# Performance work log

Measured on AMD Instinct MI355X. Metric: run time of the kernel, lower is better.

The kernel has to match this reference:

```python
import jax, jax.numpy as jnp
import numpy as np

B, S, D = 8, 1024, 1024
H, DH = 16, 64  # num_attention_heads, attention_head_size; H*DH == D


def setup_inputs() -> dict:
    key = jax.random.key(0)
    ks = jax.random.split(key, 6)
    scale = 0.02
    return {
        "hidden_states": jax.random.normal(ks[0], (B, S, D), jnp.float32),
        "right_hidden_states": jax.random.normal(ks[1], (B, S, D), jnp.float32),
        "attention_mask": jnp.ones((B, S, S), jnp.float32),
        "Wq": jax.random.normal(ks[2], (D, H * DH), jnp.float32) * scale,
        "bq": jnp.zeros((H * DH,), jnp.float32),
        "Wk": jax.random.normal(ks[3], (D, H * DH), jnp.float32) * scale,
        "bk": jnp.zeros((H * DH,), jnp.float32),
        "Wv": jax.random.normal(ks[4], (D, H * DH), jnp.float32) * scale,
        "bv": jnp.zeros((H * DH,), jnp.float32),
    }


def _split_heads(x, b):
    # (B, S, H*DH) -> (B, H, S, DH)
    return x.reshape(b, -1, H, DH).transpose(0, 2, 1, 3)


def reference(hidden_states, right_hidden_states, attention_mask, Wq, bq, Wk, bk, Wv, bv):
    b = hidden_states.shape[0]
    q = _split_heads(hidden_states @ Wq + bq, b)          # (B,H,Sq,DH)
    k = _split_heads(right_hidden_states @ Wk + bk, b)    # (B,H,Sk,DH)
    v = _split_heads(right_hidden_states @ Wv + bv, b)    # (B,H,Sk,DH)

    scores = jnp.einsum("bhqd,bhkd->bhqk", q, k) / jnp.sqrt(jnp.asarray(DH, q.dtype))
    scores = jnp.sum(scores, axis=1, keepdims=True)       # (B,1,Sq,Sk) head-summed

    ext = (1.0 - attention_mask[:, None, :, :].astype(scores.dtype)) * -1e9
    probs = jax.nn.softmax(scores + ext, axis=-1)         # (B,1,Sq,Sk)

    ctx = jnp.matmul(probs, v)                            # broadcast -> (B,H,Sq,DH)
    # Faithful to original: reshape WITHOUT transposing heads back.
    return ctx.reshape(b, -1, H * DH)                     # (B,Sq,H*DH)
```

## Files before the change

kernel.cpp:

```cpp
#include <hip/hip_runtime.h>
#include <stdint.h>

constexpr int S = 1024;
constexpr int D = 1024;
constexpr int NB = 8;

typedef __bf16 bf16x8 __attribute__((ext_vector_type(8)));
typedef float floatx4 __attribute__((ext_vector_type(4)));

#define AS1 __attribute__((address_space(1)))
#define AS3 __attribute__((address_space(3)))

__device__ __forceinline__ unsigned short f2bf(float f) {
  unsigned u = __builtin_bit_cast(unsigned, f);
  u += 0x7fffu + ((u >> 16) & 1u);
  return (unsigned short)(u >> 16);
}

__device__ __forceinline__ void gload16(const void* g, void* l) {
  __builtin_amdgcn_global_load_lds((const AS1 unsigned int*)g, (AS3 unsigned int*)l, 16, 0, 0);
}

__global__ __launch_bounds__(256) void prep_kernel(const float4* __restrict__ hs4,
                                                   const float4* __restrict__ rhs4,
                                                   ushort4* __restrict__ hsb4,
                                                   ushort4* __restrict__ rhsb4, int n4,
                                                   const float* __restrict__ Wq,
                                                   const float* __restrict__ Wk,
                                                   const float* __restrict__ Wv,
                                                   unsigned short* __restrict__ Wcat) {
  __shared__ float tile[32][33];
  const int bid = blockIdx.x;
  if (bid < 16384) {
    int i = bid * 256 + threadIdx.x;
    const float4* src;
    ushort4* dst;
    int j;
    if (i < n4) {
      src = hs4; dst = hsb4; j = i;
    } else {
      src = rhs4; dst = rhsb4; j = i - n4;
    }
    float4 v = src[j];
    ushort4 o;
    o.x = f2bf(v.x); o.y = f2bf(v.y); o.z = f2bf(v.z); o.w = f2bf(v.w);
    dst[j] = o;
  } else {
    const int t = bid - 16384;
    const int z = t >> 10;
    const int r = t & 1023;
    const float* W = (z == 0) ? Wq : (z == 1) ? Wk : Wv;
    unsigned short* Wt = Wcat + (long long)z * D * D;
    const int bx = (r & 31) * 32;
    const int by = (r >> 5) * 32;
    const int x = threadIdx.x & 31;
    const int y0 = threadIdx.x >> 5;
    for (int i = 0; i < 4; ++i) {
      int y = y0 + i * 8;
      tile[y][x] = W[(by + y) * D + bx + x];
    }
    __syncthreads();
    for (int i = 0; i < 4; ++i) {
      int y = y0 + i * 8;
      Wt[(long long)(bx + y) * D + by + x] = f2bf(tile[x][y]);
    }
  }
}


#define GEMM_STAGE_SETUP(Abase, lda_, Bbase, ldb_)                                   \
  const int lrow = w * 32 + ((tid & 63) >> 2);  \
  const int csw = (((tid & 3) ^ ((lrow >> 1) & 3)) * 8);                              \
  const unsigned short* aG0 = (Abase) + (long long)lrow * (lda_) + csw;               \
  const unsigned short* aG1 = aG0 + (long long)16 * (lda_);                           \
  const unsigned short* bG0 = (Bbase) + (long long)lrow * (ldb_) + csw;               \
  const unsigned short* bG1 = bG0 + (long long)16 * (ldb_);                           \
  unsigned short* aL0 = As + w * 1024;                                                \
  unsigned short* aL1 = As + w * 1024 + 512;                                          \
  unsigned short* bL0 = Bs + w * 1024;                                                \
  unsigned short* bL1 = Bs + w * 1024 + 512;

#define GEMM_STAGE(k0off, poff)          \
  gload16(aG0 + (k0off), aL0 + (poff));  \
  gload16(aG1 + (k0off), aL1 + (poff));  \
  gload16(bG0 + (k0off), bL0 + (poff));  \
  gload16(bG1 + (k0off), bL1 + (poff));

#define GEMM_COMPUTE(poff)                                                            \
  {                                                                                   \
    bf16x8 af[4], bfr[4];                                                             \
    for (int t = 0; t < 4; ++t) {                                                     \
      af[t] = *reinterpret_cast<const bf16x8*>(As + (poff) + (wm + t * 16 + r15) * 32 + pq); \
      bfr[t] = *reinterpret_cast<const bf16x8*>(Bs + (poff) + (wn + t * 16 + r15) * 32 + pq); \
    }                                                                                 \
    for (int mt = 0; mt < 4; ++mt)                                                    \
      for (int nt = 0; nt < 4; ++nt)                                                  \
        acc[mt][nt] =                                                                 \
            __builtin_amdgcn_mfma_f32_16x16x32_bf16(af[mt], bfr[nt], acc[mt][nt], 0, 0, 0); \
  }

__global__ __launch_bounds__(256) void gemm_qkv_kernel(
    const unsigned short* __restrict__ hsb, const unsigned short* __restrict__ rhsb,
    const unsigned short* __restrict__ Wcat, unsigned short* __restrict__ Qm,
    unsigned short* __restrict__ Km, unsigned short* __restrict__ Vmt,
    const float* __restrict__ bq, const float* __restrict__ bk, const float* __restrict__ bv) {
  __shared__ __align__(16) unsigned short As[2 * 4096];
  __shared__ __align__(16) unsigned short Bs[2 * 4096];
  const int tid = threadIdx.x;
  const int lane = tid & 63;
  const int w = tid >> 6;
  const int bid = blockIdx.x;
  const int local = bid >> 3;
  const int n_tile = (bid & 7) * 3 + (local % 3);
  const long long m0 = (long long)(local / 3) * 128;
  const long long n0g = (long long)n_tile * 128;
  const int seg = n_tile >> 3;
  const unsigned short* A = ((seg == 0) ? hsb : rhsb) + m0 * D;
  const unsigned short* Bt = Wcat + n0g * D;
  const float* bias = (seg == 0) ? bq : (seg == 1) ? bk : bv;

  GEMM_STAGE_SETUP(A, D, Bt, D)

  floatx4 zero4 = {0.f, 0.f, 0.f, 0.f};
  floatx4 acc[4][4];
  for (int i = 0; i < 4; ++i)
    for (int j = 0; j < 4; ++j) acc[i][j] = zero4;

  const int r15 = lane & 15;
  const int quad = lane >> 4;
  const int pq = (quad ^ ((r15 >> 1) & 3)) * 8;
  const int wm = (w >> 1) * 64;
  const int wn = (w & 1) * 64;

  GEMM_STAGE(0, 0)
  for (int k0 = 0; k0 < D; k0 += 64) {
    __syncthreads();
    if (k0 + 32 < D) GEMM_STAGE(k0 + 32, 4096)
    GEMM_COMPUTE(0)
    __syncthreads();
    if (k0 + 64 < D) GEMM_STAGE(k0 + 64, 0)
    GEMM_COMPUTE(4096)
  }

  const long long nloc0 = n0g & 1023;
  for (int mt = 0; mt < 4; ++mt) {
    for (int nt = 0; nt < 4; ++nt) {
      const long long mrow = m0 + wm + mt * 16 + quad * 4;
      const long long nc = nloc0 + wn + nt * 16 + r15;
      const float bval = bias[nc];
      floatx4 v = acc[mt][nt];
      for (int e = 0; e < 4; ++e) {
        float val = v[e] + bval;
        long long m = mrow + e;
        if (seg == 0) {
          Qm[m * D + nc] = f2bf(val);
        } else if (seg == 1) {
          Km[m * D + nc] = f2bf(val);
        } else {
          Vmt[(m >> 10) * (long long)(S * D) + nc * S + (m & 1023)] = f2bf(val);
        }
      }
    }
  }
}

template <int MODE>
__global__ __launch_bounds__(256) void gemm_nt_kernel(
    const unsigned short* __restrict__ A, int lda, long long strideA,
    const unsigned short* __restrict__ Bt, int ldb, long long strideB, float* __restrict__ C,
    long long strideC, float alpha, int K) {
  __shared__ __align__(16) unsigned short As[2 * 4096];
  __shared__ __align__(16) unsigned short Bs[2 * 4096];
  const int tid = threadIdx.x;
  const int lane = tid & 63;
  const int w = tid >> 6;
  const int bid = blockIdx.x;
  const int z = bid & 7;
  const int local = bid >> 3;
  const long long m0 = (long long)(local & 7) * 128;
  const long long n0 = (long long)(local >> 3) * 128;
  const unsigned short* Ab = A + (long long)z * strideA + m0 * lda;
  const unsigned short* Bb = Bt + (long long)z * strideB + n0 * ldb;

  GEMM_STAGE_SETUP(Ab, lda, Bb, ldb)

  floatx4 zero4 = {0.f, 0.f, 0.f, 0.f};
  floatx4 acc[4][4];
  for (int i = 0; i < 4; ++i)
    for (int j = 0; j < 4; ++j) acc[i][j] = zero4;

  const int r15 = lane & 15;
  const int quad = lane >> 4;
  const int pq = (quad ^ ((r15 >> 1) & 3)) * 8;
  const int wm = (w >> 1) * 64;
  const int wn = (w & 1) * 64;

  GEMM_STAGE(0, 0)
  for (int k0 = 0; k0 < K; k0 += 64) {
    __syncthreads();
    if (k0 + 32 < K) GEMM_STAGE(k0 + 32, 4096)
    GEMM_COMPUTE(0)
    __syncthreads();
    if (k0 + 64 < K) GEMM_STAGE(k0 + 64, 0)
    GEMM_COMPUTE(4096)
  }

  for (int mt = 0; mt < 4; ++mt) {
    for (int nt = 0; nt < 4; ++nt) {
      const long long mrow = m0 + wm + mt * 16 + quad * 4;
      const long long ncol = n0 + wn + nt * 16 + r15;
      floatx4 v = acc[mt][nt];
      for (int e = 0; e < 4; ++e) {
        float val = v[e] * alpha;
        long long m = mrow + e;
        if constexpr (MODE == 2) {
          C[(long long)z * strideC + m * S + ncol] = val;
        } else {
          C[(long long)z * strideC + (ncol >> 6) * (long long)(S * 64) + m * 64 + (ncol & 63)] =
              val;
        }
      }
    }
  }
}

__global__ __launch_bounds__(256) void softmax_kernel(const float* __restrict__ scores,
                                                      const float* __restrict__ mask,
                                                      unsigned short* __restrict__ probs) {
  const int bid = blockIdx.x;
  const long long row = (long long)(bid & 7) * 1024 + (bid >> 3);
  const float4* s4 = (const float4*)(scores + row * S);
  const float4* m4 = (const float4*)(mask + row * S);
  ushort4* p4 = (ushort4*)(probs + row * 1024);
  const int tid = threadIdx.x;
  const int lane = tid & 63, w = tid >> 6;
  float4 sv = s4[tid];
  float4 mv = m4[tid];
  float v[4] = {sv.x + (1.0f - mv.x) * -1e9f, sv.y + (1.0f - mv.y) * -1e9f,
                sv.z + (1.0f - mv.z) * -1e9f, sv.w + (1.0f - mv.w) * -1e9f};
  float mx = fmaxf(fmaxf(v[0], v[1]), fmaxf(v[2], v[3]));
  for (int off = 32; off; off >>= 1) mx = fmaxf(mx, __shfl_xor(mx, off, 64));
  __shared__ float redm[4], reds[4];
  if (lane == 0) redm[w] = mx;
  __syncthreads();
  mx = fmaxf(fmaxf(redm[0], redm[1]), fmaxf(redm[2], redm[3]));
  float sum = 0.f;
  for (int i = 0; i < 4; ++i) {
    v[i] = __expf(v[i] - mx);
    sum += v[i];
  }
  for (int off = 32; off; off >>= 1) sum += __shfl_xor(sum, off, 64);
  if (lane == 0) reds[w] = sum;
  __syncthreads();
  sum = reds[0] + reds[1] + reds[2] + reds[3];
  float inv = 1.0f / sum;
  ushort4 o;
  o.x = f2bf(v[0] * inv);
  o.y = f2bf(v[1] * inv);
  o.z = f2bf(v[2] * inv);
  o.w = f2bf(v[3] * inv);
  p4[tid] = o;
}

extern "C" void kernel_launch(void* const* d_in, const int* in_sizes, int n_in, void* d_out,
                              int out_size, void* d_ws, size_t ws_size, hipStream_t stream) {
  const float* hs = (const float*)d_in[0];
  const float* rhs = (const float*)d_in[1];
  const float* mask = (const float*)d_in[2];
  const float* Wq = (const float*)d_in[3];
  const float* bq = (const float*)d_in[4];
  const float* Wk = (const float*)d_in[5];
  const float* bk = (const float*)d_in[6];
  const float* Wv = (const float*)d_in[7];
  const float* bv = (const float*)d_in[8];
  float* out = (float*)d_out;
  char* ws = (char*)d_ws;
  const size_t MB = 1ull << 20;
  unsigned short* Wcat = (unsigned short*)(ws + 0 * MB);
  unsigned short* hsb = (unsigned short*)(ws + 6 * MB);
  unsigned short* rhsb = (unsigned short*)(ws + 22 * MB);
  unsigned short* Qm = (unsigned short*)(ws + 38 * MB);
  unsigned short* Km = (unsigned short*)(ws + 54 * MB);
  unsigned short* Vmt = (unsigned short*)(ws + 70 * MB);
  float* scores = (float*)(ws + 6 * MB);
  unsigned short* probs = Qm;

  const int n4 = NB * S * D / 4;
  prep_kernel<<<16384 + 3072, 256, 0, stream>>>((const float4*)hs, (const float4*)rhs,
                                                (ushort4*)hsb, (ushort4*)rhsb, n4, Wq, Wk, Wv,
                                                Wcat);

  gemm_qkv_kernel<<<1536, 256, 0, stream>>>(hsb, rhsb, Wcat, Qm, Km, Vmt, bq, bk, bv);

  gemm_nt_kernel<2><<<512, 256, 0, stream>>>(Qm, D, (long long)S * D, Km, D, (long long)S * D,
                                             scores, (long long)S * S, 0.125f, D);
  softmax_kernel<<<NB * S, 256, 0, stream>>>(scores, mask, probs);
  gemm_nt_kernel<3><<<512, 256, 0, stream>>>(probs, 1024, (long long)S * 1024, Vmt, D,
                                             (long long)S * D, out, (long long)S * D, 1.f, D);
}
```

Baseline: 326.6 us.

## Fuse mask+exp into scores GEMM, defer softmax normalization to ctx GEMM

Removes the separate softmax kernel and fp32 scores buffer. The scores GEMM epilogue now applies the scale and mask, exponentiates without max subtraction, writes bf16 exponentials, and emits per-tile partial row sums. The ctx GEMM sums those partials and scales its output by the reciprocal row sum. It also replaces the double-buffered LDS pipeline with a single-buffer load/sync/compute loop and switches to plain 2D/3D grid indexing. Dropping the row max risks overflow for large scores, and the single buffer loses load/compute overlap.

```diff
diff --git a/kernel.cpp b/kernel.cpp
--- a/kernel.cpp
+++ b/kernel.cpp
@@ -68,79 +68,70 @@
 }
 
 
-#define GEMM_STAGE_SETUP(Abase, lda_, Bbase, ldb_)                                   \
-  const int lrow = w * 32 + ((tid & 63) >> 2);  \
-  const int csw = (((tid & 3) ^ ((lrow >> 1) & 3)) * 8);                              \
-  const unsigned short* aG0 = (Abase) + (long long)lrow * (lda_) + csw;               \
-  const unsigned short* aG1 = aG0 + (long long)16 * (lda_);                           \
-  const unsigned short* bG0 = (Bbase) + (long long)lrow * (ldb_) + csw;               \
-  const unsigned short* bG1 = bG0 + (long long)16 * (ldb_);                           \
-  unsigned short* aL0 = As + w * 1024;                                                \
-  unsigned short* aL1 = As + w * 1024 + 512;                                          \
-  unsigned short* bL0 = Bs + w * 1024;                                                \
-  unsigned short* bL1 = Bs + w * 1024 + 512;
-
-#define GEMM_STAGE(k0off, poff)          \
-  gload16(aG0 + (k0off), aL0 + (poff));  \
-  gload16(aG1 + (k0off), aL1 + (poff));  \
-  gload16(bG0 + (k0off), bL0 + (poff));  \
-  gload16(bG1 + (k0off), bL1 + (poff));
-
-#define GEMM_COMPUTE(poff)                                                            \
-  {                                                                                   \
-    bf16x8 af[4], bfr[4];                                                             \
-    for (int t = 0; t < 4; ++t) {                                                     \
-      af[t] = *reinterpret_cast<const bf16x8*>(As + (poff) + (wm + t * 16 + r15) * 32 + pq); \
-      bfr[t] = *reinterpret_cast<const bf16x8*>(Bs + (poff) + (wn + t * 16 + r15) * 32 + pq); \
-    }                                                                                 \
-    for (int mt = 0; mt < 4; ++mt)                                                    \
-      for (int nt = 0; nt < 4; ++nt)                                                  \
-        acc[mt][nt] =                                                                 \
+#define GEMM_STAGE_SETUP(Abase, lda_, Bbase, ldb_)                            \
+  const int srow = tid >> 2;                                                  \
+  const int scg = (((tid & 3) ^ ((srow >> 1) & 3)) * 8);                      \
+  const unsigned short* aG0 = (Abase) + (long long)srow * (lda_) + scg;       \
+  const unsigned short* aG1 = aG0 + (long long)64 * (lda_);                   \
+  const unsigned short* bG0 = (Bbase) + (long long)srow * (ldb_) + scg;       \
+  const unsigned short* bG1 = bG0 + (long long)64 * (ldb_);                   \
+  unsigned short* aL0 = As + w * 512;                                         \
+  unsigned short* aL1 = As + w * 512 + 2048;                                  \
+  unsigned short* bL0 = Bs + w * 512;                                         \
+  unsigned short* bL1 = Bs + w * 512 + 2048;
+
+#define GEMM_KLOOP(Klen)                                                               \
+  for (int k0 = 0; k0 < (Klen); k0 += 32) {                                            \
+    gload16(aG0 + k0, aL0);                                                            \
+    gload16(aG1 + k0, aL1);                                                            \
+    gload16(bG0 + k0, bL0);                                                            \
+    gload16(bG1 + k0, bL1);                                                            \
+    __syncthreads();                                                                   \
+    bf16x8 af[4], bfr[4];                                                              \
+    for (int t = 0; t < 4; ++t) {                                                      \
+      af[t] = *reinterpret_cast<const bf16x8*>(As + (wm + t * 16 + r15) * 32 + pq);    \
+      bfr[t] = *reinterpret_cast<const bf16x8*>(Bs + (wn + t * 16 + r15) * 32 + pq);   \
+    }                                                                                  \
+    for (int mt = 0; mt < 4; ++mt)                                                     \
+      for (int nt = 0; nt < 4; ++nt)                                                   \
+        acc[mt][nt] =                                                                  \
             __builtin_amdgcn_mfma_f32_16x16x32_bf16(af[mt], bfr[nt], acc[mt][nt], 0, 0, 0); \
-  }
+    __syncthreads();                                                                   \
+  }
+
+#define GEMM_COMMON_IDX                  \
+  const int tid = threadIdx.x;           \
+  const int lane = tid & 63;             \
+  const int w = tid >> 6;                \
+  const int r15 = lane & 15;             \
+  const int quad = lane >> 4;            \
+  const int pq = (quad ^ ((r15 >> 1) & 3)) * 8; \
+  const int wm = (w >> 1) * 64;          \
+  const int wn = (w & 1) * 64;
+
+#define GEMM_ACC_INIT                    \
+  floatx4 acc[4][4];                     \
+  for (int i = 0; i < 4; ++i)            \
+    for (int j = 0; j < 4; ++j) acc[i][j] = {0.f, 0.f, 0.f, 0.f};
 
 __global__ __launch_bounds__(256) void gemm_qkv_kernel(
     const unsigned short* __restrict__ hsb, const unsigned short* __restrict__ rhsb,
     const unsigned short* __restrict__ Wcat, unsigned short* __restrict__ Qm,
     unsigned short* __restrict__ Km, unsigned short* __restrict__ Vmt,
     const float* __restrict__ bq, const float* __restrict__ bk, const float* __restrict__ bv) {
-  __shared__ __align__(16) unsigned short As[2 * 4096];
-  __shared__ __align__(16) unsigned short Bs[2 * 4096];
-  const int tid = threadIdx.x;
-  const int lane = tid & 63;
-  const int w = tid >> 6;
-  const int bid = blockIdx.x;
-  const int local = bid >> 3;
-  const int n_tile = (bid & 7) * 3 + (local % 3);
-  const long long m0 = (long long)(local / 3) * 128;
-  const long long n0g = (long long)n_tile * 128;
-  const int seg = n_tile >> 3;
+  __shared__ __align__(16) unsigned short As[128 * 32];
+  __shared__ __align__(16) unsigned short Bs[128 * 32];
+  GEMM_COMMON_IDX
+  const long long n0g = (long long)blockIdx.x * 128;
+  const int seg = (int)(n0g >> 10);
+  const long long m0 = (long long)blockIdx.y * 128;
   const unsigned short* A = ((seg == 0) ? hsb : rhsb) + m0 * D;
   const unsigned short* Bt = Wcat + n0g * D;
   const float* bias = (seg == 0) ? bq : (seg == 1) ? bk : bv;
 
   GEMM_STAGE_SETUP(A, D, Bt, D)
-
-  floatx4 zero4 = {0.f, 0.f, 0.f, 0.f};
-  floatx4 acc[4][4];
-  for (int i = 0; i < 4; ++i)
-    for (int j = 0; j < 4; ++j) acc[i][j] = zero4;
-
-  const int r15 = lane & 15;
-  const int quad = lane >> 4;
-  const int pq = (quad ^ ((r15 >> 1) & 3)) * 8;
-  const int wm = (w >> 1) * 64;
-  const int wn = (w & 1) * 64;
-
-  GEMM_STAGE(0, 0)
-  for (int k0 = 0; k0 < D; k0 += 64) {
-    __syncthreads();
-    if (k0 + 32 < D) GEMM_STAGE(k0 + 32, 4096)
-    GEMM_COMPUTE(0)
-    __syncthreads();
-    if (k0 + 64 < D) GEMM_STAGE(k0 + 64, 0)
-    GEMM_COMPUTE(4096)
-  }
+  GEMM_ACC_INIT
+  GEMM_KLOOP(D)
 
   const long long nloc0 = n0g & 1023;
   for (int mt = 0; mt < 4; ++mt) {
@@ -164,102 +155,96 @@
   }
 }
 
-template <int MODE>
-__global__ __launch_bounds__(256) void gemm_nt_kernel(
-    const unsigned short* __restrict__ A, int lda, long long strideA,
-    const unsigned short* __restrict__ Bt, int ldb, long long strideB, float* __restrict__ C,
-    long long strideC, float alpha, int K) {
-  __shared__ __align__(16) unsigned short As[2 * 4096];
-  __shared__ __align__(16) unsigned short Bs[2 * 4096];
-  const int tid = threadIdx.x;
-  const int lane = tid & 63;
-  const int w = tid >> 6;
-  const int bid = blockIdx.x;
-  const int z = bid & 7;
-  const int local = bid >> 3;
-  const long long m0 = (long long)(local & 7) * 128;
-  const long long n0 = (long long)(local >> 3) * 128;
-  const unsigned short* Ab = A + (long long)z * strideA + m0 * lda;
-  const unsigned short* Bb = Bt + (long long)z * strideB + n0 * ldb;
-
-  GEMM_STAGE_SETUP(Ab, lda, Bb, ldb)
-
-  floatx4 zero4 = {0.f, 0.f, 0.f, 0.f};
-  floatx4 acc[4][4];
-  for (int i = 0; i < 4; ++i)
-    for (int j = 0; j < 4; ++j) acc[i][j] = zero4;
-
-  const int r15 = lane & 15;
-  const int quad = lane >> 4;
-  const int pq = (quad ^ ((r15 >> 1) & 3)) * 8;
-  const int wm = (w >> 1) * 64;
-  const int wn = (w & 1) * 64;
-
-  GEMM_STAGE(0, 0)
-  for (int k0 = 0; k0 < K; k0 += 64) {
-    __syncthreads();
-    if (k0 + 32 < K) GEMM_STAGE(k0 + 32, 4096)
-    GEMM_COMPUTE(0)
-    __syncthreads();
-    if (k0 + 64 < K) GEMM_STAGE(k0 + 64, 0)
-    GEMM_COMPUTE(4096)
-  }
+__global__ __launch_bounds__(256) void gemm_scores_kernel(
+    const unsigned short* __restrict__ Qm, const unsigned short* __restrict__ Km,
+    const float* __restrict__ mask, unsigned short* __restrict__ E,
+    float* __restrict__ rowsumP) {
+  __shared__ __align__(16) unsigned short As[128 * 32];
+  __shared__ __align__(16) unsigned short Bs[128 * 32];
+  GEMM_COMMON_IDX
+  const int z = blockIdx.z;
+  const long long m0 = (long long)blockIdx.y * 128;
+  const long long n0 = (long long)blockIdx.x * 128;
+  const unsigned short* A = Qm + (long long)z * S * D + m0 * D;
+  const unsigned short* Bt = Km + (long long)z * S * D + n0 * D;
+
+  GEMM_STAGE_SETUP(A, D, Bt, D)
+  GEMM_ACC_INIT
+  GEMM_KLOOP(D)
+
+  const long long zE = (long long)z * S * 1024;
+  float rowpart[4][4];
+  for (int mt = 0; mt < 4; ++mt)
+    for (int e = 0; e < 4; ++e) rowpart[mt][e] = 0.f;
 
   for (int mt = 0; mt < 4; ++mt) {
     for (int nt = 0; nt < 4; ++nt) {
       const long long mrow = m0 + wm + mt * 16 + quad * 4;
+      const long long nc = n0 + wn + nt * 16 + r15;
+      floatx4 v = acc[mt][nt];
+      for (int e = 0; e < 4; ++e) {
+        long long m = mrow + e;
+        float mval = mask[zE + m * 1024 + nc];
+        float sc = v[e] * 0.125f + (1.0f - mval) * -1e9f;
+        float Ev = __expf(sc);
+        E[zE + m * 1024 + nc] = f2bf(Ev);
+        rowpart[mt][e] += Ev;
+      }
+    }
+  }
+  const int slot = ((int)blockIdx.x << 11) + ((wn >> 6) << 10);
+  for (int mt = 0; mt < 4; ++mt) {
+    for (int e = 0; e < 4; ++e) {
+      float s = rowpart[mt][e];
+      s += __shfl_xor(s, 1, 64);
+      s += __shfl_xor(s, 2, 64);
+      s += __shfl_xor(s, 4, 64);
+      s += __shfl_xor(s, 8, 64);
+      if (r15 == 0) {
+        int mloc = (int)(m0 + wm + mt * 16 + quad * 4 + e);
+        rowsumP[(z << 14) + slot + mloc] = s;
+      }
+    }
+  }
+}
+
+__global__ __launch_bounds__(256) void gemm_ctx_kernel(const unsigned short* __restrict__ E,
+                                                       const unsigned short* __restrict__ Vmt,
+                                                       const float* __restrict__ rowsumP,
+                                                       float* __restrict__ out) {
+  __shared__ __align__(16) unsigned short As[128 * 32];
+  __shared__ __align__(16) unsigned short Bs[128 * 32];
+  __shared__ float rsinv[128];
+  GEMM_COMMON_IDX
+  const int z = blockIdx.z;
+  const long long m0 = (long long)blockIdx.y * 128;
+  const long long n0 = (long long)blockIdx.x * 128;
+  const unsigned short* A = E + (long long)z * S * 1024 + m0 * 1024;
+  const unsigned short* Bt = Vmt + (long long)z * S * D + n0 * D;
+
+  if (tid < 128) {
+    float s = 0.f;
+    for (int t = 0; t < 16; ++t) s += rowsumP[(z << 14) + (t << 10) + (int)m0 + tid];
+    rsinv[tid] = 1.0f / s;
+  }
+
+  GEMM_STAGE_SETUP(A, 1024, Bt, D)
+  GEMM_ACC_INIT
+  GEMM_KLOOP(1024)
+
+  for (int mt = 0; mt < 4; ++mt) {
+    for (int nt = 0; nt < 4; ++nt) {
+      const int r0 = wm + mt * 16 + quad * 4;
       const long long ncol = n0 + wn + nt * 16 + r15;
       floatx4 v = acc[mt][nt];
       for (int e = 0; e < 4; ++e) {
-        float val = v[e] * alpha;
-        long long m = mrow + e;
-        if constexpr (MODE == 2) {
-          C[(long long)z * strideC + m * S + ncol] = val;
-        } else {
-          C[(long long)z * strideC + (ncol >> 6) * (long long)(S * 64) + m * 64 + (ncol & 63)] =
-              val;
-        }
-      }
-    }
-  }
-}
-
-__global__ __launch_bounds__(256) void softmax_kernel(const float* __restrict__ scores,
-                                                      const float* __restrict__ mask,
-                                                      unsigned short* __restrict__ probs) {
-  const int bid = blockIdx.x;
-  const long long row = (long long)(bid & 7) * 1024 + (bid >> 3);
-  const float4* s4 = (const float4*)(scores + row * S);
-  const float4* m4 = (const float4*)(mask + row * S);
-  ushort4* p4 = (ushort4*)(probs + row * 1024);
-  const int tid = threadIdx.x;
-  const int lane = tid & 63, w = tid >> 6;
-  float4 sv = s4[tid];
-  float4 mv = m4[tid];
-  float v[4] = {sv.x + (1.0f - mv.x) * -1e9f, sv.y + (1.0f - mv.y) * -1e9f,
-                sv.z + (1.0f - mv.z) * -1e9f, sv.w + (1.0f - mv.w) * -1e9f};
-  float mx = fmaxf(fmaxf(v[0], v[1]), fmaxf(v[2], v[3]));
-  for (int off = 32; off; off >>= 1) mx = fmaxf(mx, __shfl_xor(mx, off, 64));
-  __shared__ float redm[4], reds[4];
-  if (lane == 0) redm[w] = mx;
-  __syncthreads();
-  mx = fmaxf(fmaxf(redm[0], redm[1]), fmaxf(redm[2], redm[3]));
-  float sum = 0.f;
-  for (int i = 0; i < 4; ++i) {
-    v[i] = __expf(v[i] - mx);
-    sum += v[i];
-  }
-  for (int off = 32; off; off >>= 1) sum += __shfl_xor(sum, off, 64);
-  if (lane == 0) reds[w] = sum;
-  __syncthreads();
-  sum = reds[0] + reds[1] + reds[2] + reds[3];
-  float inv = 1.0f / sum;
-  ushort4 o;
-  o.x = f2bf(v[0] * inv);
-  o.y = f2bf(v[1] * inv);
-  o.z = f2bf(v[2] * inv);
-  o.w = f2bf(v[3] * inv);
-  p4[tid] = o;
+        long long m = m0 + r0 + e;
+        float val = v[e] * rsinv[r0 + e];
+        out[(long long)z * S * D + (ncol >> 6) * (long long)(S * 64) + m * 64 + (ncol & 63)] =
+            val;
+      }
+    }
+  }
 }
 
 extern "C" void kernel_launch(void* const* d_in, const int* in_sizes, int n_in, void* d_out,
@@ -282,19 +267,17 @@
   unsigned short* Qm = (unsigned short*)(ws + 38 * MB);
   unsigned short* Km = (unsigned short*)(ws + 54 * MB);
   unsigned short* Vmt = (unsigned short*)(ws + 70 * MB);
-  float* scores = (float*)(ws + 6 * MB);
-  unsigned short* probs = Qm;
+  unsigned short* E = (unsigned short*)(ws + 6 * MB);
+  float* rowsumP = (float*)(ws + 22 * MB);
 
   const int n4 = NB * S * D / 4;
   prep_kernel<<<16384 + 3072, 256, 0, stream>>>((const float4*)hs, (const float4*)rhs,
                                                 (ushort4*)hsb, (ushort4*)rhsb, n4, Wq, Wk, Wv,
                                                 Wcat);
 
-  gemm_qkv_kernel<<<1536, 256, 0, stream>>>(hsb, rhsb, Wcat, Qm, Km, Vmt, bq, bk, bv);
-
-  gemm_nt_kernel<2><<<512, 256, 0, stream>>>(Qm, D, (long long)S * D, Km, D, (long long)S * D,
-                                             scores, (long long)S * S, 0.125f, D);
-  softmax_kernel<<<NB * S, 256, 0, stream>>>(scores, mask, probs);
-  gemm_nt_kernel<3><<<512, 256, 0, stream>>>(probs, 1024, (long long)S * 1024, Vmt, D,
-                                             (long long)S * D, out, (long long)S * D, 1.f, D);
-}
+  gemm_qkv_kernel<<<dim3(24, 64), 256, 0, stream>>>(hsb, rhsb, Wcat, Qm, Km, Vmt, bq, bk, bv);
+
+  gemm_scores_kernel<<<dim3(8, 8, NB), 256, 0, stream>>>(Qm, Km, mask, E, rowsumP);
+
+  gemm_ctx_kernel<<<dim3(8, 8, NB), 256, 0, stream>>>(E, Vmt, rowsumP, out);
+}
```

Result: faster. 300.6 us (-8.0%).
